# Performance work log

Hardware: AMD Instinct MI355X
Metric: run time of the kernel (lower is better)

Reference implementation:

```python
import jax, jax.numpy as jnp
import numpy as np

L, B, Q, D = 6, 2, 300, 256  # levels, batch, num queries, embed dim


def setup_inputs() -> dict:
    key = jax.random.key(0)
    ks = jax.random.split(key, 20)
    s = 1.0 / np.sqrt(D)
    s2 = 1.0 / np.sqrt(2 * D)
    inp = {
        "hs": jax.random.normal(ks[0], (L, B, Q, D), jnp.float32),
        # per-level proj_q / proj_k (Linear(D, D) cloned L times)
        "Wq": jax.random.uniform(ks[1], (L, D, D), jnp.float32, -s, s),
        "bq": jax.random.uniform(ks[2], (L, D), jnp.float32, -s, s),
        "Wk": jax.random.uniform(ks[3], (L, D, D), jnp.float32, -s, s),
        "bk": jax.random.uniform(ks[4], (L, D), jnp.float32, -s, s),
        # final subject/object projections on hs[-1]
        "Wsub": jax.random.uniform(ks[5], (D, D), jnp.float32, -s, s),
        "bsub": jax.random.uniform(ks[6], (D,), jnp.float32, -s, s),
        "Wobj": jax.random.uniform(ks[7], (D, D), jnp.float32, -s, s),
        "bobj": jax.random.uniform(ks[8], (D,), jnp.float32, -s, s),
        # gate: Linear(2D, 1)
        "Wg": jax.random.uniform(ks[9], (2 * D, 1), jnp.float32, -s2, s2),
        "bg": jax.random.uniform(ks[10], (1,), jnp.float32, -s2, s2),
        # MLPHEAD: 2D -> D -> D -> 1
        "W1": jax.random.uniform(ks[11], (2 * D, D), jnp.float32, -s2, s2),
        "b1": jax.random.uniform(ks[12], (D,), jnp.float32, -s2, s2),
        "W2": jax.random.uniform(ks[13], (D, D), jnp.float32, -s, s),
        "b2": jax.random.uniform(ks[14], (D,), jnp.float32, -s, s),
        "W3": jax.random.uniform(ks[15], (D, 1), jnp.float32, -s, s),
        "b3": jax.random.uniform(ks[16], (1,), jnp.float32, -s, s),
    }
    return inp


def reference(hs, Wq, bq, Wk, bk, Wsub, bsub, Wobj, bobj, Wg, bg, W1, b1, W2, b2, W3, b3):
    l, b, q, d = hs.shape
    # per-level projections: [L, B, Q, D]
    Qs = jnp.einsum('lbqd,lde->lbqe', hs, Wq) + bq[:, None, None, :]
    Ks = jnp.einsum('lbqd,lde->lbqe', hs, Wk) + bk[:, None, None, :]
    # extra (L+1)-th level from final sub/obj projections of hs[-1]
    sub = hs[-1] @ Wsub + bsub  # [B, Q, D]
    obj = hs[-1] @ Wobj + bobj
    Q_all = jnp.concatenate([Qs, sub[None]], axis=0)  # [L+1, B, Q, D]
    K_all = jnp.concatenate([Ks, obj[None]], axis=0)
    # gate logit for pair (i, j) at level m = wa.q_m[i] + wb.k_m[j] + bg,
    # identical math to sigmoid(Linear(cat([q_i, k_j]))) without materializing
    # the [B, Q, Q, L+1, 2D] broadcast tensor.
    wa, wb = Wg[:d, 0], Wg[d:, 0]
    gq = jnp.einsum('lbqd,d->lbq', Q_all, wa)  # [L+1, B, Q]
    gk = jnp.einsum('lbqd,d->lbq', K_all, wb)
    gate = jax.nn.sigmoid(gq[:, :, :, None] + gk[:, :, None, :] + bg[0])  # [L+1, B, Qi, Qj]
    # gated sum over levels; query half depends on i, key half on j
    out_q = jnp.einsum('lbij,lbid->bijd', gate, Q_all)  # [B, Q, Q, D]
    out_k = jnp.einsum('lbij,lbjd->bijd', gate, K_all)
    gated = jnp.concatenate([out_q, out_k], axis=-1)  # [B, Q, Q, 2D]
    # rel predictor MLP: 2D -> D -> D -> 1
    x = jax.nn.relu(gated @ W1 + b1)
    x = jax.nn.relu(x @ W2 + b2)
    pred = (x @ W3 + b3)[..., 0]  # [B, Q, Q]
    pred_rel = jnp.broadcast_to(pred[None], (l,) + pred.shape)  # [L, B, Q, Q]
    return pred_rel
```

## Files before the change

### kernel.cpp

```cpp
#include <hip/hip_runtime.h>


typedef _Float16 half8 __attribute__((ext_vector_type(8)));
typedef _Float16 half4v __attribute__((ext_vector_type(4)));
typedef float floatx4 __attribute__((ext_vector_type(4)));

#define MFMA16(a, b, c) __builtin_amdgcn_mfma_f32_16x16x32_f16((a), (b), (c), 0, 0, 0)

__global__ __launch_bounds__(256) void k_wprep(
    const float* __restrict__ Wq, const float* __restrict__ Wk,
    const float* __restrict__ Wsub, const float* __restrict__ Wobj,
    const float* __restrict__ W1, _Float16* __restrict__ WT)
{
    int eid = blockIdx.x * 256 + threadIdx.x;
    int mat = eid >> 13;
    int rem = eid & 8191;
    int tileid = rem >> 6;
    int lane = rem & 63;
    const float* src;
    if      (mat < 6)  src = Wq + mat * 65536;
    else if (mat < 12) src = Wk + (mat - 6) * 65536;
    else if (mat == 12) src = Wsub;
    else if (mat == 13) src = Wobj;
    else if (mat == 14) src = W1;
    else               src = W1 + 65536;
    int nb = tileid >> 3, kb = tileid & 7;
    int n = nb * 16 + (lane & 15);
    int k = kb * 32 + (lane >> 4) * 8;
    half8 h;
    #pragma unroll
    for (int j = 0; j < 8; ++j) h[j] = (_Float16)src[(k + j) * 256 + n];
    *(half8*)(WT + mat * 65536 + tileid * 512 + lane * 8) = h;
}

__global__ __launch_bounds__(256) void k_projpq(
    const float* __restrict__ hs, _Float16* __restrict__ WT,
    const float* __restrict__ bq, const float* __restrict__ bk,
    const float* __restrict__ bsub, const float* __restrict__ bobj,
    const float* __restrict__ Wg, const float* __restrict__ W2,
    _Float16* __restrict__ PQt, _Float16* __restrict__ PKt,
    float* __restrict__ g_ws)
{
    int t = threadIdx.x;
    if (blockIdx.x >= 532) {
        int eid = (blockIdx.x - 532) * 256 + t;
        int tileid = eid >> 6, lane = eid & 63;
        int nb = tileid >> 3, kb = tileid & 7;
        int n = nb * 16 + (lane & 15);
        int k = kb * 32 + (lane >> 4) * 8;
        half8 h;
        #pragma unroll
        for (int j = 0; j < 8; ++j) h[j] = (_Float16)W2[(k + j) * 256 + n];
        *(half8*)(WT + 16 * 65536 + tileid * 512 + lane * 8) = h;
        return;
    }

    __shared__ __align__(16) _Float16 Ah[16][264];
    __shared__ __align__(16) _Float16 Xb[16][264];

    int lane = t & 63, wv = t >> 6;
    int mr = lane & 15, hf = lane >> 4;
    int u = blockIdx.x;
    int s = u / 19, rt = u - s * 19;
    int m0 = rt * 16;
    int qk = s & 1, rr = s >> 1;
    int l = rr % 7, b = rr / 7;
    int hs_l = (l < 6) ? l : 5;
    const float* src = hs + (hs_l * 2 + b) * 76800;
    int projmat = (l < 6) ? (qk * 6 + l) : (12 + qk);
    const _Float16* WprojT = WT + projmat * 65536;
    const _Float16* W1hT = WT + (14 + qk) * 65536;
    const float* bias = (l < 6) ? ((qk ? bk : bq) + l * 256) : (qk ? bobj : bsub);
    _Float16* dstP = qk ? PKt : PQt;
    const float* wvec = Wg + qk * 256;
    float* gdst = g_ws + qk * 4200 + (l * 2 + b) * 300;

    {
        int row = t >> 4, qt = t & 15;
        int m = m0 + row; if (m > 299) m = 299;
        const float* pp = src + m * 256 + qt * 16;
        #pragma unroll
        for (int i = 0; i < 4; ++i) {
            float4 v = *(const float4*)(pp + 4 * i);
            half4v h;
            h[0] = (_Float16)v.x; h[1] = (_Float16)v.y;
            h[2] = (_Float16)v.z; h[3] = (_Float16)v.w;
            *(half4v*)&Ah[row][qt * 16 + 4 * i] = h;
        }
    }
    __syncthreads();

    floatx4 acc[4];
    #pragma unroll
    for (int i = 0; i < 4; ++i) acc[i] = floatx4{0.f, 0.f, 0.f, 0.f};
    #pragma unroll
    for (int ks = 0; ks < 8; ++ks) {
        half8 bfr = *(const half8*)&Ah[mr][ks * 32 + hf * 8];
        #pragma unroll
        for (int mt = 0; mt < 4; ++mt) {
            half8 afr = *(const half8*)(WprojT + (((wv * 4 + mt) * 8 + ks) << 9) + lane * 8);
            acc[mt] = MFMA16(afr, bfr, acc[mt]);
        }
    }
    #pragma unroll
    for (int mt = 0; mt < 4; ++mt) {
        int n0 = wv * 64 + mt * 16 + hf * 4;
        float4 bb = *(const float4*)&bias[n0];
        float bv[4] = {bb.x, bb.y, bb.z, bb.w};
        half4v h;
        #pragma unroll
        for (int u2 = 0; u2 < 4; ++u2) h[u2] = (_Float16)(acc[mt][u2] + bv[u2]);
        *(half4v*)&Xb[mr][n0] = h;
    }
    __syncthreads();

    {
        int row = t >> 4, qt = t & 15;
        half8 x0 = *(const half8*)&Xb[row][qt * 16];
        half8 x1 = *(const half8*)&Xb[row][qt * 16 + 8];
        const float* wp = wvec + qt * 16;
        float sum = 0.f;
        #pragma unroll
        for (int i = 0; i < 8; ++i) sum += (float)x0[i] * wp[i];
        #pragma unroll
        for (int i = 0; i < 8; ++i) sum += (float)x1[i] * wp[8 + i];
        sum += __shfl_xor(sum, 1);
        sum += __shfl_xor(sum, 2);
        sum += __shfl_xor(sum, 4);
        sum += __shfl_xor(sum, 8);
        int m = m0 + row;
        if (qt == 0 && m < 300) gdst[m] = sum;
    }

    floatx4 acc2[4];
    #pragma unroll
    for (int i = 0; i < 4; ++i) acc2[i] = floatx4{0.f, 0.f, 0.f, 0.f};
    #pragma unroll
    for (int ks = 0; ks < 8; ++ks) {
        half8 bfr = *(const half8*)&Xb[mr][ks * 32 + hf * 8];
        #pragma unroll
        for (int mt = 0; mt < 4; ++mt) {
            half8 afr = *(const half8*)(W1hT + (((wv * 4 + mt) * 8 + ks) << 9) + lane * 8);
            acc2[mt] = MFMA16(afr, bfr, acc2[mt]);
        }
    }
    #pragma unroll
    for (int mt = 0; mt < 4; ++mt) {
        int n0 = wv * 64 + mt * 16 + hf * 4;
        half4v h;
        #pragma unroll
        for (int u2 = 0; u2 < 4; ++u2) h[u2] = (_Float16)acc2[mt][u2];
        *(half4v*)&Ah[mr][n0] = h;
    }
    __syncthreads();

    #pragma unroll
    for (int z = 0; z < 2; ++z) {
        int it = rt * 2 + z;
        int n = t;
        half8 h;
        #pragma unroll
        for (int io = 0; io < 8; ++io) h[io] = Ah[z * 8 + io][n];
        *(half8*)(dstP + ((size_t)((b * 38 + it) * 7 + l) * 256 + n) * 8) = h;
    }
}

__global__ __launch_bounds__(256, 4) void k_fused(
    const _Float16* __restrict__ PQt, const _Float16* __restrict__ PKt,
    const float* __restrict__ g_ws, const float* __restrict__ b1,
    const _Float16* __restrict__ W2T, const float* __restrict__ b2,
    const float* __restrict__ W3, const float* __restrict__ b3,
    const float* __restrict__ bg, float* __restrict__ out)
{
    union SM {
        _Float16 Pt[256][72];
        _Float16 X[64][264];
    };
    __shared__ __align__(16) SM sm;
    __shared__ float gate[7][64];

    int t = threadIdx.x, lane = t & 63, wv = t >> 6;
    int mr = lane & 15, hf = lane >> 4;
    int bid = blockIdx.x;
    int b = bid / 1444, rem = bid - b * 1444;
    int it = rem / 38, jt = rem - it * 38;
    int i0 = it * 8, j0 = jt * 8;

    const _Float16* baseQ = PQt + ((size_t)((b * 38 + it) * 7) * 256 + t) * 8;
    const _Float16* baseK = PKt + ((size_t)((b * 38 + jt) * 7) * 256 + t) * 8;
    half8 pq[7], pk[7];
    #pragma unroll
    for (int l = 0; l < 7; ++l) pq[l] = *(const half8*)(baseQ + l * 2048);
    #pragma unroll
    for (int l = 0; l < 7; ++l) pk[l] = *(const half8*)(baseK + l * 2048);

    float bg0 = bg[0];
    for (int task = t; task < 448; task += 256) {
        int l = task >> 6, row = task & 63;
        int i = i0 + (row >> 3); if (i > 299) i = 299;
        int j = j0 + (row & 7);  if (j > 299) j = 299;
        float z = g_ws[l * 600 + b * 300 + i] + g_ws[4200 + l * 600 + b * 300 + j] + bg0;
        gate[l][row] = 1.0f / (1.0f + __expf(-z));
    }

    #pragma unroll
    for (int l = 0; l < 7; ++l)
        *(half8*)&sm.Pt[t][l * 8] = pq[l];
    *(half8*)&sm.Pt[t][56] = half8{};
    __syncthreads();

    floatx4 acc1[4][4];
    #pragma unroll
    for (int i = 0; i < 4; ++i)
        #pragma unroll
        for (int j = 0; j < 4; ++j) acc1[i][j] = floatx4{0.f, 0.f, 0.f, 0.f};

    #pragma unroll
    for (int ktl = 0; ktl < 2; ++ktl) {
        int l = ktl * 4 + hf;
        half8 bfr[4];
        #pragma unroll
        for (int nt = 0; nt < 4; ++nt) {
            int r = nt * 16 + mr;
            float g = (l < 7) ? gate[l][r] : 0.f;
            _Float16 gh = (_Float16)g;
            const _Float16 hz = (_Float16)0.f;
            half8 f = {};
            f[nt * 2]     = (mr < 8)  ? gh : hz;
            f[nt * 2 + 1] = (mr >= 8) ? gh : hz;
            bfr[nt] = f;
        }
        #pragma unroll
        for (int mt = 0; mt < 4; ++mt) {
            half8 afr = *(const half8*)&sm.Pt[wv * 64 + mt * 16 + mr][ktl * 32 + hf * 8];
            #pragma unroll
            for (int nt = 0; nt < 4; ++nt)
                acc1[mt][nt] = MFMA16(afr, bfr[nt], acc1[mt][nt]);
        }
    }
    __syncthreads();

    #pragma unroll
    for (int l = 0; l < 7; ++l)
        *(half8*)&sm.Pt[t][l * 8] = pk[l];
    __syncthreads();

    #pragma unroll
    for (int ktl = 0; ktl < 2; ++ktl) {
        int l = ktl * 4 + hf;
        half8 bfr[4];
        #pragma unroll
        for (int nt = 0; nt < 4; ++nt) {
            int r = nt * 16 + mr;
            float g = (l < 7) ? gate[l][r] : 0.f;
            _Float16 gh = (_Float16)g;
            const _Float16 hz = (_Float16)0.f;
            half8 f = {};
            #pragma unroll
            for (int j = 0; j < 8; ++j)
                f[j] = (j == (mr & 7)) ? gh : hz;
            bfr[nt] = f;
        }
        #pragma unroll
        for (int mt = 0; mt < 4; ++mt) {
            half8 afr = *(const half8*)&sm.Pt[wv * 64 + mt * 16 + mr][ktl * 32 + hf * 8];
            #pragma unroll
            for (int nt = 0; nt < 4; ++nt)
                acc1[mt][nt] = MFMA16(afr, bfr[nt], acc1[mt][nt]);
        }
    }
    __syncthreads();

    #pragma unroll
    for (int mt = 0; mt < 4; ++mt) {
        int n0 = wv * 64 + mt * 16 + hf * 4;
        float4 bb = *(const float4*)&b1[n0];
        float bv[4] = {bb.x, bb.y, bb.z, bb.w};
        #pragma unroll
        for (int nt = 0; nt < 4; ++nt) {
            int r = nt * 16 + mr;
            half4v h;
            #pragma unroll
            for (int u = 0; u < 4; ++u) {
                float v = acc1[mt][nt][u] + bv[u];
                h[u] = (_Float16)(v > 0.f ? v : 0.f);
            }
            *(half4v*)&sm.X[r][n0] = h;
        }
    }
    __syncthreads();

    floatx4 acc2[4][4];
    #pragma unroll
    for (int i = 0; i < 4; ++i)
        #pragma unroll
        for (int j = 0; j < 4; ++j) acc2[i][j] = floatx4{0.f, 0.f, 0.f, 0.f};
    for (int s = 0; s < 8; ++s) {
        half8 bfr[4];
        #pragma unroll
        for (int nt = 0; nt < 4; ++nt)
            bfr[nt] = *(const half8*)&sm.X[nt * 16 + mr][s * 32 + hf * 8];
        #pragma unroll
        for (int mt = 0; mt < 4; ++mt) {
            half8 afr = *(const half8*)(W2T + (((wv * 4 + mt) * 8 + s) << 9) + lane * 8);
            #pragma unroll
            for (int nt = 0; nt < 4; ++nt)
                acc2[mt][nt] = MFMA16(afr, bfr[nt], acc2[mt][nt]);
        }
    }

    {
        float* red = &gate[0][0];
        float p[4] = {0.f, 0.f, 0.f, 0.f};
        #pragma unroll
        for (int mt = 0; mt < 4; ++mt) {
            int n0 = wv * 64 + mt * 16 + hf * 4;
            float4 bb = *(const float4*)&b2[n0];
            float4 w3 = *(const float4*)&W3[n0];
            float bv[4] = {bb.x, bb.y, bb.z, bb.w};
            float wv3[4] = {w3.x, w3.y, w3.z, w3.w};
            #pragma unroll
            for (int nt = 0; nt < 4; ++nt)
                #pragma unroll
                for (int u = 0; u < 4; ++u) {
                    float v = acc2[mt][nt][u] + bv[u];
                    v = v > 0.f ? v : 0.f;
                    p[nt] += v * wv3[u];
                }
        }
        #pragma unroll
        for (int nt = 0; nt < 4; ++nt) {
            p[nt] += __shfl_xor(p[nt], 16);
            p[nt] += __shfl_xor(p[nt], 32);
        }
        if (hf == 0) {
            #pragma unroll
            for (int nt = 0; nt < 4; ++nt)
                red[wv * 64 + nt * 16 + mr] = p[nt];
        }
        __syncthreads();
        if (t < 64) {
            float pred = red[t] + red[64 + t] + red[128 + t] + red[192 + t] + b3[0];
            int i = i0 + (t >> 3), j = j0 + (t & 7);
            if (i < 300 && j < 300) {
                int base = b * 90000 + i * 300 + j;
                #pragma unroll
                for (int lo = 0; lo < 6; ++lo) out[lo * 180000 + base] = pred;
            }
        }
    }
}

extern "C" void kernel_launch(void* const* d_in, const int* in_sizes, int n_in,
                              void* d_out, int out_size, void* d_ws, size_t ws_size,
                              hipStream_t stream) {
    (void)in_sizes; (void)n_in; (void)out_size; (void)ws_size;
    const float* hs   = (const float*)d_in[0];
    const float* Wq   = (const float*)d_in[1];
    const float* bq   = (const float*)d_in[2];
    const float* Wk   = (const float*)d_in[3];
    const float* bk   = (const float*)d_in[4];
    const float* Wsub = (const float*)d_in[5];
    const float* bsub = (const float*)d_in[6];
    const float* Wobj = (const float*)d_in[7];
    const float* bobj = (const float*)d_in[8];
    const float* Wg   = (const float*)d_in[9];
    const float* bg   = (const float*)d_in[10];
    const float* W1   = (const float*)d_in[11];
    const float* b1   = (const float*)d_in[12];
    const float* W2   = (const float*)d_in[13];
    const float* b2   = (const float*)d_in[14];
    const float* W3   = (const float*)d_in[15];
    const float* b3   = (const float*)d_in[16];

    char* ws = (char*)d_ws;
    float* g_ws   = (float*)ws;
    _Float16* WT  = (_Float16*)(ws + 33600);
    _Float16* PQt = WT + 17 * 65536;
    _Float16* PKt = PQt + 1089536;

    k_wprep<<<512, 256, 0, stream>>>(Wq, Wk, Wsub, Wobj, W1, WT);
    k_projpq<<<564, 256, 0, stream>>>(hs, WT, bq, bk, bsub, bobj, Wg, W2,
                                      PQt, PKt, g_ws);
    k_fused<<<2888, 256, 0, stream>>>(PQt, PKt, g_ws, b1, WT + 16 * 65536,
                                      b2, W3, b3, bg, (float*)d_out);
}
```

Baseline: 145.5 us.

## Shrink fused kernel LDS with XOR-swizzled unpadded layout and raise occupancy

```diff
diff --git a/kernel.cpp b/kernel.cpp
--- a/kernel.cpp
+++ b/kernel.cpp
@@ -165,19 +165,14 @@
     }
 }
 
-__global__ __launch_bounds__(256, 4) void k_fused(
+__global__ __launch_bounds__(256, 5) void k_fused(
     const _Float16* __restrict__ PQt, const _Float16* __restrict__ PKt,
     const float* __restrict__ g_ws, const float* __restrict__ b1,
     const _Float16* __restrict__ W2T, const float* __restrict__ b2,
     const float* __restrict__ W3, const float* __restrict__ b3,
     const float* __restrict__ bg, float* __restrict__ out)
 {
-    union SM {
-        _Float16 Pt[256][72];
-        _Float16 X[64][264];
-    };
-    __shared__ __align__(16) SM sm;
-    __shared__ float gate[7][64];
+    __shared__ __align__(16) _Float16 smh[16384];
 
     int t = threadIdx.x, lane = t & 63, wv = t >> 6;
     int mr = lane & 15, hf = lane >> 4;
@@ -194,19 +189,22 @@
     #pragma unroll
     for (int l = 0; l < 7; ++l) pk[l] = *(const half8*)(baseK + l * 2048);
 
+    if (t < 64) smh[((t * 8 + (7 ^ (t & 7))) << 3) + 7] = (_Float16)0.f;
+    else        *(half8*)&smh[(t * 8 + (7 ^ (t & 7))) << 3] = half8{};
+
     float bg0 = bg[0];
     for (int task = t; task < 448; task += 256) {
         int l = task >> 6, row = task & 63;
         int i = i0 + (row >> 3); if (i > 299) i = 299;
         int j = j0 + (row & 7);  if (j > 299) j = 299;
         float z = g_ws[l * 600 + b * 300 + i] + g_ws[4200 + l * 600 + b * 300 + j] + bg0;
-        gate[l][row] = 1.0f / (1.0f + __expf(-z));
+        smh[((row * 8 + (7 ^ (row & 7))) << 3) + l] =
+            (_Float16)(1.0f / (1.0f + __expf(-z)));
     }
 
     #pragma unroll
     for (int l = 0; l < 7; ++l)
-        *(half8*)&sm.Pt[t][l * 8] = pq[l];
-    *(half8*)&sm.Pt[t][56] = half8{};
+        *(half8*)&smh[(t * 8 + (l ^ (t & 7))) << 3] = pq[l];
     __syncthreads();
 
     floatx4 acc1[4][4];
@@ -222,8 +220,7 @@
         #pragma unroll
         for (int nt = 0; nt < 4; ++nt) {
             int r = nt * 16 + mr;
-            float g = (l < 7) ? gate[l][r] : 0.f;
-            _Float16 gh = (_Float16)g;
+            _Float16 gh = smh[((r * 8 + (7 ^ (r & 7))) << 3) + l];
             const _Float16 hz = (_Float16)0.f;
             half8 f = {};
             f[nt * 2]     = (mr < 8)  ? gh : hz;
@@ -232,7 +229,8 @@
         }
         #pragma unroll
         for (int mt = 0; mt < 4; ++mt) {
-            half8 afr = *(const half8*)&sm.Pt[wv * 64 + mt * 16 + mr][ktl * 32 + hf * 8];
+            int row = wv * 64 + mt * 16 + mr;
+            half8 afr = *(const half8*)&smh[(row * 8 + ((ktl * 4 + hf) ^ (row & 7))) << 3];
             #pragma unroll
             for (int nt = 0; nt < 4; ++nt)
                 acc1[mt][nt] = MFMA16(afr, bfr[nt], acc1[mt][nt]);
@@ -242,7 +240,7 @@
 
     #pragma unroll
     for (int l = 0; l < 7; ++l)
-        *(half8*)&sm.Pt[t][l * 8] = pk[l];
+        *(half8*)&smh[(t * 8 + (l ^ (t & 7))) << 3] = pk[l];
     __syncthreads();
 
     #pragma unroll
@@ -252,8 +250,7 @@
         #pragma unroll
         for (int nt = 0; nt < 4; ++nt) {
             int r = nt * 16 + mr;
-            float g = (l < 7) ? gate[l][r] : 0.f;
-            _Float16 gh = (_Float16)g;
+            _Float16 gh = smh[((r * 8 + (7 ^ (r & 7))) << 3) + l];
             const _Float16 hz = (_Float16)0.f;
             half8 f = {};
             #pragma unroll
@@ -263,7 +260,8 @@
         }
         #pragma unroll
         for (int mt = 0; mt < 4; ++mt) {
-            half8 afr = *(const half8*)&sm.Pt[wv * 64 + mt * 16 + mr][ktl * 32 + hf * 8];
+            int row = wv * 64 + mt * 16 + mr;
+            half8 afr = *(const half8*)&smh[(row * 8 + ((ktl * 4 + hf) ^ (row & 7))) << 3];
             #pragma unroll
             for (int nt = 0; nt < 4; ++nt)
                 acc1[mt][nt] = MFMA16(afr, bfr[nt], acc1[mt][nt]);
@@ -285,7 +283,7 @@
                 float v = acc1[mt][nt][u] + bv[u];
                 h[u] = (_Float16)(v > 0.f ? v : 0.f);
             }
-            *(half4v*)&sm.X[r][n0] = h;
+            *(half4v*)&smh[((r * 32 + ((n0 >> 3) ^ (r & 7))) << 3) + (n0 & 7)] = h;
         }
     }
     __syncthreads();
@@ -298,8 +296,10 @@
     for (int s = 0; s < 8; ++s) {
         half8 bfr[4];
         #pragma unroll
-        for (int nt = 0; nt < 4; ++nt)
-            bfr[nt] = *(const half8*)&sm.X[nt * 16 + mr][s * 32 + hf * 8];
+        for (int nt = 0; nt < 4; ++nt) {
+            int r = nt * 16 + mr;
+            bfr[nt] = *(const half8*)&smh[(r * 32 + ((s * 4 + hf) ^ (r & 7))) << 3];
+        }
         #pragma unroll
         for (int mt = 0; mt < 4; ++mt) {
             half8 afr = *(const half8*)(W2T + (((wv * 4 + mt) * 8 + s) << 9) + lane * 8);
@@ -310,7 +310,6 @@
     }
 
     {
-        float* red = &gate[0][0];
         float p[4] = {0.f, 0.f, 0.f, 0.f};
         #pragma unroll
         for (int mt = 0; mt < 4; ++mt) {
@@ -333,6 +332,8 @@
             p[nt] += __shfl_xor(p[nt], 16);
             p[nt] += __shfl_xor(p[nt], 32);
         }
+        __syncthreads();
+        float* red = (float*)smh;
         if (hf == 0) {
             #pragma unroll
             for (int nt = 0; nt < 4; ++nt)
```

Measured after the change: 279.0 us. 1.92x slower.

## Split fused MLP block across 8 waves with half the output tile each

Applied to the files above, without the earlier changes.

```diff
diff --git a/kernel.cpp b/kernel.cpp
--- a/kernel.cpp
+++ b/kernel.cpp
@@ -165,7 +165,7 @@
     }
 }
 
-__global__ __launch_bounds__(256, 4) void k_fused(
+__global__ __launch_bounds__(512, 5) void k_fused(
     const _Float16* __restrict__ PQt, const _Float16* __restrict__ PKt,
     const float* __restrict__ g_ws, const float* __restrict__ b1,
     const _Float16* __restrict__ W2T, const float* __restrict__ b2,
@@ -186,32 +186,36 @@
     int it = rem / 38, jt = rem - it * 38;
     int i0 = it * 8, j0 = jt * 8;
 
-    const _Float16* baseQ = PQt + ((size_t)((b * 38 + it) * 7) * 256 + t) * 8;
-    const _Float16* baseK = PKt + ((size_t)((b * 38 + jt) * 7) * 256 + t) * 8;
-    half8 pq[7], pk[7];
-    #pragma unroll
-    for (int l = 0; l < 7; ++l) pq[l] = *(const half8*)(baseQ + l * 2048);
-    #pragma unroll
-    for (int l = 0; l < 7; ++l) pk[l] = *(const half8*)(baseK + l * 2048);
+    half8 pf[7];
+    {
+        int row = t & 255;
+        const _Float16* basep = (t < 256)
+            ? PQt + ((size_t)((b * 38 + it) * 7) * 256 + row) * 8
+            : PKt + ((size_t)((b * 38 + jt) * 7) * 256 + row) * 8;
+        #pragma unroll
+        for (int l = 0; l < 7; ++l) pf[l] = *(const half8*)(basep + l * 2048);
+    }
 
     float bg0 = bg[0];
-    for (int task = t; task < 448; task += 256) {
-        int l = task >> 6, row = task & 63;
+    if (t < 448) {
+        int l = t >> 6, row = t & 63;
         int i = i0 + (row >> 3); if (i > 299) i = 299;
         int j = j0 + (row & 7);  if (j > 299) j = 299;
         float z = g_ws[l * 600 + b * 300 + i] + g_ws[4200 + l * 600 + b * 300 + j] + bg0;
         gate[l][row] = 1.0f / (1.0f + __expf(-z));
     }
 
-    #pragma unroll
-    for (int l = 0; l < 7; ++l)
-        *(half8*)&sm.Pt[t][l * 8] = pq[l];
-    *(half8*)&sm.Pt[t][56] = half8{};
-    __syncthreads();
-
-    floatx4 acc1[4][4];
-    #pragma unroll
-    for (int i = 0; i < 4; ++i)
+    if (t < 256) {
+        #pragma unroll
+        for (int l = 0; l < 7; ++l)
+            *(half8*)&sm.Pt[t][l * 8] = pf[l];
+        *(half8*)&sm.Pt[t][56] = half8{};
+    }
+    __syncthreads();
+
+    floatx4 acc1[2][4];
+    #pragma unroll
+    for (int i = 0; i < 2; ++i)
         #pragma unroll
         for (int j = 0; j < 4; ++j) acc1[i][j] = floatx4{0.f, 0.f, 0.f, 0.f};
 
@@ -231,8 +235,8 @@
             bfr[nt] = f;
         }
         #pragma unroll
-        for (int mt = 0; mt < 4; ++mt) {
-            half8 afr = *(const half8*)&sm.Pt[wv * 64 + mt * 16 + mr][ktl * 32 + hf * 8];
+        for (int mt = 0; mt < 2; ++mt) {
+            half8 afr = *(const half8*)&sm.Pt[wv * 32 + mt * 16 + mr][ktl * 32 + hf * 8];
             #pragma unroll
             for (int nt = 0; nt < 4; ++nt)
                 acc1[mt][nt] = MFMA16(afr, bfr[nt], acc1[mt][nt]);
@@ -240,11 +244,18 @@
     }
     __syncthreads();
 
-    #pragma unroll
-    for (int l = 0; l < 7; ++l)
-        *(half8*)&sm.Pt[t][l * 8] = pk[l];
-    __syncthreads();
-
+    if (t >= 256) {
+        int row = t & 255;
+        #pragma unroll
+        for (int l = 0; l < 7; ++l)
+            *(half8*)&sm.Pt[row][l * 8] = pf[l];
+    }
+    __syncthreads();
+
+    half8 oh;
+    #pragma unroll
+    for (int j = 0; j < 8; ++j)
+        oh[j] = (j == (mr & 7)) ? (_Float16)1.0f : (_Float16)0.f;
     #pragma unroll
     for (int ktl = 0; ktl < 2; ++ktl) {
         int l = ktl * 4 + hf;
@@ -254,16 +265,14 @@
             int r = nt * 16 + mr;
             float g = (l < 7) ? gate[l][r] : 0.f;
             _Float16 gh = (_Float16)g;
-            const _Float16 hz = (_Float16)0.f;
-            half8 f = {};
-            #pragma unroll
-            for (int j = 0; j < 8; ++j)
-                f[j] = (j == (mr & 7)) ? gh : hz;
-            bfr[nt] = f;
-        }
-        #pragma unroll
-        for (int mt = 0; mt < 4; ++mt) {
-            half8 afr = *(const half8*)&sm.Pt[wv * 64 + mt * 16 + mr][ktl * 32 + hf * 8];
+            half8 gh8;
+            #pragma unroll
+            for (int j = 0; j < 8; ++j) gh8[j] = gh;
+            bfr[nt] = oh * gh8;
+        }
+        #pragma unroll
+        for (int mt = 0; mt < 2; ++mt) {
+            half8 afr = *(const half8*)&sm.Pt[wv * 32 + mt * 16 + mr][ktl * 32 + hf * 8];
             #pragma unroll
             for (int nt = 0; nt < 4; ++nt)
                 acc1[mt][nt] = MFMA16(afr, bfr[nt], acc1[mt][nt]);
@@ -272,8 +281,8 @@
     __syncthreads();
 
     #pragma unroll
-    for (int mt = 0; mt < 4; ++mt) {
-        int n0 = wv * 64 + mt * 16 + hf * 4;
+    for (int mt = 0; mt < 2; ++mt) {
+        int n0 = wv * 32 + mt * 16 + hf * 4;
         float4 bb = *(const float4*)&b1[n0];
         float bv[4] = {bb.x, bb.y, bb.z, bb.w};
         #pragma unroll
@@ -290,9 +299,9 @@
     }
     __syncthreads();
 
-    floatx4 acc2[4][4];
-    #pragma unroll
-    for (int i = 0; i < 4; ++i)
+    floatx4 acc2[2][4];
+    #pragma unroll
+    for (int i = 0; i < 2; ++i)
         #pragma unroll
         for (int j = 0; j < 4; ++j) acc2[i][j] = floatx4{0.f, 0.f, 0.f, 0.f};
     for (int s = 0; s < 8; ++s) {
@@ -301,8 +310,8 @@
         for (int nt = 0; nt < 4; ++nt)
             bfr[nt] = *(const half8*)&sm.X[nt * 16 + mr][s * 32 + hf * 8];
         #pragma unroll
-        for (int mt = 0; mt < 4; ++mt) {
-            half8 afr = *(const half8*)(W2T + (((wv * 4 + mt) * 8 + s) << 9) + lane * 8);
+        for (int mt = 0; mt < 2; ++mt) {
+            half8 afr = *(const half8*)(W2T + (((wv * 2 + mt) * 8 + s) << 9) + lane * 8);
             #pragma unroll
             for (int nt = 0; nt < 4; ++nt)
                 acc2[mt][nt] = MFMA16(afr, bfr[nt], acc2[mt][nt]);
@@ -310,11 +319,10 @@
     }
 
     {
-        float* red = &gate[0][0];
         float p[4] = {0.f, 0.f, 0.f, 0.f};
         #pragma unroll
-        for (int mt = 0; mt < 4; ++mt) {
-            int n0 = wv * 64 + mt * 16 + hf * 4;
+        for (int mt = 0; mt < 2; ++mt) {
+            int n0 = wv * 32 + mt * 16 + hf * 4;
             float4 bb = *(const float4*)&b2[n0];
             float4 w3 = *(const float4*)&W3[n0];
             float bv[4] = {bb.x, bb.y, bb.z, bb.w};
@@ -333,6 +341,8 @@
             p[nt] += __shfl_xor(p[nt], 16);
             p[nt] += __shfl_xor(p[nt], 32);
         }
+        __syncthreads();
+        float* red = (float*)&sm.X[0][0];
         if (hf == 0) {
             #pragma unroll
             for (int nt = 0; nt < 4; ++nt)
@@ -340,7 +350,9 @@
         }
         __syncthreads();
         if (t < 64) {
-            float pred = red[t] + red[64 + t] + red[128 + t] + red[192 + t] + b3[0];
+            float pred = b3[0];
+            #pragma unroll
+            for (int w = 0; w < 8; ++w) pred += red[w * 64 + t];
             int i = i0 + (t >> 3), j = j0 + (t & 7);
             if (i < 300 && j < 300) {
                 int base = b * 90000 + i * 300 + j;
@@ -382,6 +394,6 @@
     k_wprep<<<512, 256, 0, stream>>>(Wq, Wk, Wsub, Wobj, W1, WT);
     k_projpq<<<564, 256, 0, stream>>>(hs, WT, bq, bk, bsub, bobj, Wg, W2,
                                       PQt, PKt, g_ws);
-    k_fused<<<2888, 256, 0, stream>>>(PQt, PKt, g_ws, b1, WT + 16 * 65536,
+    k_fused<<<2888, 512, 0, stream>>>(PQt, PKt, g_ws, b1, WT + 16 * 65536,
                                       b2, W3, b3, bg, (float*)d_out);
 }
```

After: 145.3 us. No clear change (-0.1%).

## Load P tile MFMA fragments straight from global, dropping LDS staging

Applied to the files above, without the earlier changes.

```diff
diff --git a/kernel.cpp b/kernel.cpp
--- a/kernel.cpp
+++ b/kernel.cpp
@@ -172,11 +172,7 @@
     const float* __restrict__ W3, const float* __restrict__ b3,
     const float* __restrict__ bg, float* __restrict__ out)
 {
-    union SM {
-        _Float16 Pt[256][72];
-        _Float16 X[64][264];
-    };
-    __shared__ __align__(16) SM sm;
+    __shared__ __align__(16) _Float16 X[64][264];
     __shared__ float gate[7][64];
 
     int t = threadIdx.x, lane = t & 63, wv = t >> 6;
@@ -186,13 +182,18 @@
     int it = rem / 38, jt = rem - it * 38;
     int i0 = it * 8, j0 = jt * 8;
 
-    const _Float16* baseQ = PQt + ((size_t)((b * 38 + it) * 7) * 256 + t) * 8;
-    const _Float16* baseK = PKt + ((size_t)((b * 38 + jt) * 7) * 256 + t) * 8;
-    half8 pq[7], pk[7];
-    #pragma unroll
-    for (int l = 0; l < 7; ++l) pq[l] = *(const half8*)(baseQ + l * 2048);
-    #pragma unroll
-    for (int l = 0; l < 7; ++l) pk[l] = *(const half8*)(baseK + l * 2048);
+    const _Float16* tQ = PQt + (size_t)((b * 38 + it) * 7) * 2048;
+    const _Float16* tK = PKt + (size_t)((b * 38 + jt) * 7) * 2048;
+    int l0 = hf;
+    int l1 = (hf == 3) ? 6 : 4 + hf;
+
+    half8 afrQ[2][4];
+    #pragma unroll
+    for (int mt = 0; mt < 4; ++mt) {
+        size_t nb8 = (size_t)((wv * 64 + mt * 16 + mr) * 8);
+        afrQ[0][mt] = *(const half8*)(tQ + l0 * 2048 + nb8);
+        afrQ[1][mt] = *(const half8*)(tQ + l1 * 2048 + nb8);
+    }
 
     float bg0 = bg[0];
     for (int task = t; task < 448; task += 256) {
@@ -202,11 +203,6 @@
         float z = g_ws[l * 600 + b * 300 + i] + g_ws[4200 + l * 600 + b * 300 + j] + bg0;
         gate[l][row] = 1.0f / (1.0f + __expf(-z));
     }
-
-    #pragma unroll
-    for (int l = 0; l < 7; ++l)
-        *(half8*)&sm.Pt[t][l * 8] = pq[l];
-    *(half8*)&sm.Pt[t][56] = half8{};
     __syncthreads();
 
     floatx4 acc1[4][4];
@@ -215,46 +211,63 @@
         #pragma unroll
         for (int j = 0; j < 4; ++j) acc1[i][j] = floatx4{0.f, 0.f, 0.f, 0.f};
 
-    #pragma unroll
-    for (int ktl = 0; ktl < 2; ++ktl) {
-        int l = ktl * 4 + hf;
+    const _Float16 hz = (_Float16)0.f;
+
+    {
         half8 bfr[4];
         #pragma unroll
         for (int nt = 0; nt < 4; ++nt) {
             int r = nt * 16 + mr;
-            float g = (l < 7) ? gate[l][r] : 0.f;
-            _Float16 gh = (_Float16)g;
-            const _Float16 hz = (_Float16)0.f;
+            _Float16 gh = (_Float16)gate[l0][r];
             half8 f = {};
             f[nt * 2]     = (mr < 8)  ? gh : hz;
             f[nt * 2 + 1] = (mr >= 8) ? gh : hz;
             bfr[nt] = f;
         }
         #pragma unroll
-        for (int mt = 0; mt < 4; ++mt) {
-            half8 afr = *(const half8*)&sm.Pt[wv * 64 + mt * 16 + mr][ktl * 32 + hf * 8];
-            #pragma unroll
-            for (int nt = 0; nt < 4; ++nt)
-                acc1[mt][nt] = MFMA16(afr, bfr[nt], acc1[mt][nt]);
-        }
-    }
-    __syncthreads();
-
-    #pragma unroll
-    for (int l = 0; l < 7; ++l)
-        *(half8*)&sm.Pt[t][l * 8] = pk[l];
-    __syncthreads();
-
-    #pragma unroll
-    for (int ktl = 0; ktl < 2; ++ktl) {
-        int l = ktl * 4 + hf;
+        for (int mt = 0; mt < 4; ++mt)
+            #pragma unroll
+            for (int nt = 0; nt < 4; ++nt)
+                acc1[mt][nt] = MFMA16(afrQ[0][mt], bfr[nt], acc1[mt][nt]);
+    }
+
+    half8 afrK0[4];
+    #pragma unroll
+    for (int mt = 0; mt < 4; ++mt)
+        afrK0[mt] = *(const half8*)(tK + l0 * 2048
+                                    + (size_t)((wv * 64 + mt * 16 + mr) * 8));
+
+    {
         half8 bfr[4];
         #pragma unroll
         for (int nt = 0; nt < 4; ++nt) {
             int r = nt * 16 + mr;
-            float g = (l < 7) ? gate[l][r] : 0.f;
-            _Float16 gh = (_Float16)g;
-            const _Float16 hz = (_Float16)0.f;
+            float g = (hf < 3) ? gate[4 + hf][r] : ((hf == 3) ? 0.f : gate[4 + hf][r]);
+            _Float16 gh = (_Float16)((hf == 3) ? 0.f : g);
+            half8 f = {};
+            f[nt * 2]     = (mr < 8)  ? gh : hz;
+            f[nt * 2 + 1] = (mr >= 8) ? gh : hz;
+            bfr[nt] = f;
+        }
+        #pragma unroll
+        for (int mt = 0; mt < 4; ++mt)
+            #pragma unroll
+            for (int nt = 0; nt < 4; ++nt)
+                acc1[mt][nt] = MFMA16(afrQ[1][mt], bfr[nt], acc1[mt][nt]);
+    }
+
+    half8 afrK1[4];
+    #pragma unroll
+    for (int mt = 0; mt < 4; ++mt)
+        afrK1[mt] = *(const half8*)(tK + l1 * 2048
+                                    + (size_t)((wv * 64 + mt * 16 + mr) * 8));
+
+    {
+        half8 bfr[4];
+        #pragma unroll
+        for (int nt = 0; nt < 4; ++nt) {
+            int r = nt * 16 + mr;
+            _Float16 gh = (_Float16)gate[l0][r];
             half8 f = {};
             #pragma unroll
             for (int j = 0; j < 8; ++j)
@@ -262,14 +275,30 @@
             bfr[nt] = f;
         }
         #pragma unroll
-        for (int mt = 0; mt < 4; ++mt) {
-            half8 afr = *(const half8*)&sm.Pt[wv * 64 + mt * 16 + mr][ktl * 32 + hf * 8];
-            #pragma unroll
-            for (int nt = 0; nt < 4; ++nt)
-                acc1[mt][nt] = MFMA16(afr, bfr[nt], acc1[mt][nt]);
-        }
-    }
-    __syncthreads();
+        for (int mt = 0; mt < 4; ++mt)
+            #pragma unroll
+            for (int nt = 0; nt < 4; ++nt)
+                acc1[mt][nt] = MFMA16(afrK0[mt], bfr[nt], acc1[mt][nt]);
+    }
+
+    {
+        half8 bfr[4];
+        #pragma unroll
+        for (int nt = 0; nt < 4; ++nt) {
+            int r = nt * 16 + mr;
+            _Float16 gh = (hf == 3) ? hz : (_Float16)gate[4 + hf][r];
+            half8 f = {};
+            #pragma unroll
+            for (int j = 0; j < 8; ++j)
+                f[j] = (j == (mr & 7)) ? gh : hz;
+            bfr[nt] = f;
+        }
+        #pragma unroll
+        for (int mt = 0; mt < 4; ++mt)
+            #pragma unroll
+            for (int nt = 0; nt < 4; ++nt)
+                acc1[mt][nt] = MFMA16(afrK1[mt], bfr[nt], acc1[mt][nt]);
+    }
 
     #pragma unroll
     for (int mt = 0; mt < 4; ++mt) {
@@ -285,7 +314,7 @@
                 float v = acc1[mt][nt][u] + bv[u];
                 h[u] = (_Float16)(v > 0.f ? v : 0.f);
             }
-            *(half4v*)&sm.X[r][n0] = h;
+            *(half4v*)&X[r][n0] = h;
         }
     }
     __syncthreads();
@@ -299,7 +328,7 @@
         half8 bfr[4];
         #pragma unroll
         for (int nt = 0; nt < 4; ++nt)
-            bfr[nt] = *(const half8*)&sm.X[nt * 16 + mr][s * 32 + hf * 8];
+            bfr[nt] = *(const half8*)&X[nt * 16 + mr][s * 32 + hf * 8];
         #pragma unroll
         for (int mt = 0; mt < 4; ++mt) {
             half8 afr = *(const half8*)(W2T + (((wv * 4 + mt) * 8 + s) << 9) + lane * 8);
```

Result: no change. 147.3 us (+1.2%).
